# Kernel tuning notes

Hardware: AMD Instinct MI355X
Metric: run time of the kernel (lower is better)

## Reference

```python
import jax, jax.numpy as jnp
import numpy as np

IN_FEATURES = 4096
OUT_FEATURES = 4096
B, S = 4, 2048


def setup_inputs() -> dict:
    key = jax.random.key(0)
    k_x, k_w, k_ws, k_ss, k_b = jax.random.split(key, 5)
    x = jax.random.normal(k_x, (B, S, IN_FEATURES), dtype=jnp.float32)
    weight_quantized = jax.random.randint(k_w, (OUT_FEATURES, IN_FEATURES), -128, 128, dtype=jnp.int32).astype(jnp.int8)
    # realistic per-output-channel weight scales (small positive)
    weight_scale = jax.random.uniform(k_ws, (OUT_FEATURES,), dtype=jnp.float32, minval=1e-3, maxval=2e-2)
    # smoothing scales near 1 (clamped to [0.01, 100] in from_float)
    smooth_scale = jax.random.uniform(k_ss, (IN_FEATURES,), dtype=jnp.float32, minval=0.5, maxval=2.0)
    bias = 0.01 * jax.random.normal(k_b, (OUT_FEATURES,), dtype=jnp.float32)
    return {"x": x, "weight_quantized": weight_quantized, "weight_scale": weight_scale,
            "smooth_scale": smooth_scale, "bias": bias}


def reference(x, weight_quantized, weight_scale, smooth_scale, bias):
    # per-tensor dynamic activation quantization after smooth-scale divide
    x_smooth = x / smooth_scale                                   # [B,S,in]
    act_scale = jnp.max(jnp.abs(x_smooth)) / 127.0                # scalar
    x_quant = jnp.clip(jnp.round(x_smooth / (act_scale + 1e-5)), -128, 127).astype(jnp.int8)
    # int8 GEMM emulated in fp32 (matches torch reference: F.linear on float casts)
    out = jnp.einsum('bsi,oi->bso', x_quant.astype(jnp.float32),
                     weight_quantized.astype(jnp.float32))        # [B,S,out]
    out = out * act_scale * weight_scale                          # fused dequant
    return out + bias
```

## Files before the change

kernel.cpp:

```cpp
#include <hip/hip_runtime.h>
#include <stdint.h>

#define M_TOT 8192
#define N_TOT 4096
#define K_TOT 4096

typedef int v4i __attribute__((ext_vector_type(4)));

#define BM 256
#define BN 256
#define SUB 64
#define NS (K_TOT / SUB)
#define A_SUB (BM * SUB)
#define B_SUB (BN * SUB)
#define BUF_BYTES (A_SUB + B_SUB)

__global__ void prep_reduce(const int4* __restrict__ w32, int* __restrict__ w8,
                            int nw4, const float* __restrict__ smooth,
                            float* __restrict__ rcp, const float4* __restrict__ x,
                            unsigned int* __restrict__ maxbits, int nx4) {
  if (blockIdx.x == 0) {
    for (int i = threadIdx.x; i < K_TOT; i += blockDim.x) rcp[i] = 1.0f / smooth[i];
  }
  const int stride = gridDim.x * blockDim.x;
  const int g0 = blockIdx.x * blockDim.x + threadIdx.x;
  for (int i = g0; i < nw4; i += stride) {
    int4 v = w32[i];
    w8[i] = (v.x & 0xff) | ((v.y & 0xff) << 8) | ((v.z & 0xff) << 16) | (v.w << 24);
  }
  const float4* smooth4 = (const float4*)smooth;
  float m = 0.0f;
  for (int i = g0; i < nx4; i += stride) {
    float4 v = x[i];
    float4 s = smooth4[i & (K_TOT / 4 - 1)];
    m = fmaxf(m, fabsf(v.x / s.x));
    m = fmaxf(m, fabsf(v.y / s.y));
    m = fmaxf(m, fabsf(v.z / s.z));
    m = fmaxf(m, fabsf(v.w / s.w));
  }
#pragma unroll
  for (int off = 32; off; off >>= 1) m = fmaxf(m, __shfl_xor(m, off));
  __shared__ float sm[4];
  if ((threadIdx.x & 63) == 0) sm[threadIdx.x >> 6] = m;
  __syncthreads();
  if (threadIdx.x == 0) {
    float mm = fmaxf(fmaxf(sm[0], sm[1]), fmaxf(sm[2], sm[3]));
    atomicMax(maxbits, __float_as_uint(mm));
  }
}

__global__ void quantize_x(const float4* __restrict__ x,
                           const float4* __restrict__ rcp4,
                           const unsigned int* __restrict__ maxbits,
                           int* __restrict__ xq, int n4) {
  const float d = __uint_as_float(*maxbits) / 127.0f + 1e-5f;
  const float inv = 1.0f / d;
  int stride = gridDim.x * blockDim.x;
  for (int i = blockIdx.x * blockDim.x + threadIdx.x; i < n4; i += stride) {
    float4 v = x[i];
    float4 r = rcp4[i & (K_TOT / 4 - 1)];
    int q0 = (int)fminf(fmaxf(rintf(v.x * r.x * inv), -128.0f), 127.0f);
    int q1 = (int)fminf(fmaxf(rintf(v.y * r.y * inv), -128.0f), 127.0f);
    int q2 = (int)fminf(fmaxf(rintf(v.z * r.z * inv), -128.0f), 127.0f);
    int q3 = (int)fminf(fmaxf(rintf(v.w * r.w * inv), -128.0f), 127.0f);
    xq[i] = (q0 & 0xff) | ((q1 & 0xff) << 8) | ((q2 & 0xff) << 16) | (q3 << 24);
  }
}

__global__ __launch_bounds__(512, 2) void gemm_i8(
    const int8_t* __restrict__ Aq,
    const int8_t* __restrict__ Wt,
    const unsigned int* __restrict__ maxbits,
    const float* __restrict__ wscale,
    const float* __restrict__ bias,
    float* __restrict__ out) {
  __shared__ int8_t lds[4 * BUF_BYTES];

  const int tid = threadIdx.x;
  const int lane = tid & 63;
  const int wid = tid >> 6;
  const int l16 = lane & 15;
  const int lhi = lane >> 4;

  const int flat = blockIdx.y * gridDim.x + blockIdx.x;
  const int swz = (flat & 7) * 64 + (flat >> 3);
  const int m0 = (swz / (N_TOT / BN)) * BM;
  const int n0 = (swz % (N_TOT / BN)) * BN;

  const int wave_m = wid >> 2;
  const int wave_n = wid & 3;

  const int row_l = lane >> 2;
  const int gcol = ((lane & 3) ^ ((lane >> 3) & 3)) << 4;
  const int8_t* Abase = Aq + (size_t)m0 * K_TOT;
  const int8_t* Bbase = Wt + (size_t)n0 * K_TOT;
  int goff[2];
#pragma unroll
  for (int c = 0; c < 2; ++c) {
    int grow = (wid * 2 + c) * 16 + row_l;
    goff[c] = grow * K_TOT + gcol;
  }

  auto stage = [&](int dstbuf, int koff) {
#pragma unroll
    for (int c = 0; c < 2; ++c) {
      __builtin_amdgcn_global_load_lds(
          (const __attribute__((address_space(1))) void*)(Abase + goff[c] + koff),
          (__attribute__((address_space(3))) void*)(lds + dstbuf * BUF_BYTES + (wid * 2 + c) * 1024),
          16, 0, 0);
      __builtin_amdgcn_global_load_lds(
          (const __attribute__((address_space(1))) void*)(Bbase + goff[c] + koff),
          (__attribute__((address_space(3))) void*)(lds + dstbuf * BUF_BYTES + A_SUB + (wid * 2 + c) * 1024),
          16, 0, 0);
    }
  };

  const int slot = (lhi ^ ((l16 >> 1) & 3)) << 4;
  const int aOff = (wave_m * 128 + l16) * SUB + slot;
  const int bOff = (wave_n * 64 + l16) * SUB + slot;

  stage(0, 0);
  stage(1, SUB);
  stage(2, 2 * SUB);
  asm volatile("s_waitcnt vmcnt(8)" ::: "memory");
  __builtin_amdgcn_s_barrier();
  __builtin_amdgcn_sched_barrier(0);

  v4i acc[8][4] = {};

#pragma unroll 4
  for (int s = 0; s < NS; ++s) {
    const int buf = s & 3;
    const int8_t* Ab = lds + buf * BUF_BYTES;
    const int8_t* Bb = Ab + A_SUB;

    const int ts = (s + 3 < NS) ? (s + 3) : (NS - 1);
    stage((s + 3) & 3, ts * SUB);

    v4i a[8], b[4];
#pragma unroll
    for (int i = 0; i < 8; ++i) a[i] = *(const v4i*)(Ab + aOff + i * 1024);
#pragma unroll
    for (int j = 0; j < 4; ++j) b[j] = *(const v4i*)(Bb + bOff + j * 1024);

    __builtin_amdgcn_s_setprio(1);
#pragma unroll
    for (int i = 0; i < 8; ++i)
#pragma unroll
      for (int j = 0; j < 4; ++j)
        acc[i][j] = __builtin_amdgcn_mfma_i32_16x16x64_i8(a[i], b[j], acc[i][j], 0, 0, 0);
    __builtin_amdgcn_s_setprio(0);
    __builtin_amdgcn_sched_barrier(0);

    asm volatile("s_waitcnt lgkmcnt(0)" ::: "memory");
    asm volatile("s_waitcnt vmcnt(8)" ::: "memory");
    __builtin_amdgcn_sched_barrier(0);
    __builtin_amdgcn_s_barrier();
    __builtin_amdgcn_sched_barrier(0);
  }

  const float ascale = __uint_as_float(*maxbits) / 127.0f;
#pragma unroll
  for (int i = 0; i < 8; ++i) {
    const int orow = m0 + wave_m * 128 + i * 16 + lhi * 4;
#pragma unroll
    for (int j = 0; j < 4; ++j) {
      const int ocol = n0 + wave_n * 64 + j * 16 + l16;
      const float wsc = wscale[ocol] * ascale;
      const float bb = bias[ocol];
#pragma unroll
      for (int r = 0; r < 4; ++r) {
        out[(size_t)(orow + r) * N_TOT + ocol] = (float)acc[i][j][r] * wsc + bb;
      }
    }
  }
}

extern "C" void kernel_launch(void* const* d_in, const int* in_sizes, int n_in,
                              void* d_out, int out_size, void* d_ws, size_t ws_size,
                              hipStream_t stream) {
  const float* x = (const float*)d_in[0];
  const int* w32 = (const int*)d_in[1];
  const float* wscale = (const float*)d_in[2];
  const float* smooth = (const float*)d_in[3];
  const float* bias = (const float*)d_in[4];
  float* out = (float*)d_out;

  unsigned int* maxbits = (unsigned int*)d_ws;
  float* rcp = (float*)((char*)d_ws + 1024);
  int8_t* xq = (int8_t*)d_ws + (1 << 20);
  int8_t* wq8 = xq + (size_t)M_TOT * K_TOT;

  hipMemsetAsync(d_ws, 0, 4, stream);

  const int nw4 = N_TOT * K_TOT / 4;
  const int n4 = M_TOT * K_TOT / 4;
  prep_reduce<<<2048, 256, 0, stream>>>((const int4*)w32, (int*)wq8, nw4,
                                        smooth, rcp, (const float4*)x,
                                        maxbits, n4);
  quantize_x<<<2048, 256, 0, stream>>>((const float4*)x, (const float4*)rcp,
                                       maxbits, (int*)xq, n4);

  dim3 grid(N_TOT / BN, M_TOT / BM);
  gemm_i8<<<grid, 512, 0, stream>>>(xq, wq8, maxbits, wscale, bias, out);
}
```

Measured before the change: 224.9 us.

## Switch GEMM to 32x32x32 int8 MFMA and hoist smooth reciprocals per thread

The int8 GEMM now uses 32x32x32 MFMA instructions with 16-register accumulators in place of 16x16x64 tiles. Each wave issues fewer, larger MFMAs and reads A and B fragments as two k-halves per 64-wide sub-tile, with the epilogue store mapping adjusted to match. The prep and quantize kernels rely on the grid stride being a multiple of K/4, so each thread loads its smooth-scale values once, computes reciprocals up front, and drops the separate rcp buffer. Using a multiply by a reciprocal instead of a divide can change rounding near quantization boundaries, and the larger MFMA shape changes LDS read patterns and bank behaviour.

```diff
diff --git a/kernel.cpp b/kernel.cpp
--- a/kernel.cpp
+++ b/kernel.cpp
@@ -6,6 +6,7 @@
 #define K_TOT 4096
 
 typedef int v4i __attribute__((ext_vector_type(4)));
+typedef int v16i __attribute__((ext_vector_type(16)));
 
 #define BM 256
 #define BN 256
@@ -16,27 +17,24 @@
 #define BUF_BYTES (A_SUB + B_SUB)
 
 __global__ void prep_reduce(const int4* __restrict__ w32, int* __restrict__ w8,
-                            int nw4, const float* __restrict__ smooth,
-                            float* __restrict__ rcp, const float4* __restrict__ x,
+                            int nw4, const float4* __restrict__ smooth4,
+                            const float4* __restrict__ x,
                             unsigned int* __restrict__ maxbits, int nx4) {
-  if (blockIdx.x == 0) {
-    for (int i = threadIdx.x; i < K_TOT; i += blockDim.x) rcp[i] = 1.0f / smooth[i];
-  }
   const int stride = gridDim.x * blockDim.x;
   const int g0 = blockIdx.x * blockDim.x + threadIdx.x;
   for (int i = g0; i < nw4; i += stride) {
     int4 v = w32[i];
     w8[i] = (v.x & 0xff) | ((v.y & 0xff) << 8) | ((v.z & 0xff) << 16) | (v.w << 24);
   }
-  const float4* smooth4 = (const float4*)smooth;
+  float4 s = smooth4[g0 & (K_TOT / 4 - 1)];
+  const float rx = 1.0f / s.x, ry = 1.0f / s.y, rz = 1.0f / s.z, rw = 1.0f / s.w;
   float m = 0.0f;
   for (int i = g0; i < nx4; i += stride) {
     float4 v = x[i];
-    float4 s = smooth4[i & (K_TOT / 4 - 1)];
-    m = fmaxf(m, fabsf(v.x / s.x));
-    m = fmaxf(m, fabsf(v.y / s.y));
-    m = fmaxf(m, fabsf(v.z / s.z));
-    m = fmaxf(m, fabsf(v.w / s.w));
+    m = fmaxf(m, fabsf(v.x * rx));
+    m = fmaxf(m, fabsf(v.y * ry));
+    m = fmaxf(m, fabsf(v.z * rz));
+    m = fmaxf(m, fabsf(v.w * rw));
   }
 #pragma unroll
   for (int off = 32; off; off >>= 1) m = fmaxf(m, __shfl_xor(m, off));
@@ -50,19 +48,21 @@
 }
 
 __global__ void quantize_x(const float4* __restrict__ x,
-                           const float4* __restrict__ rcp4,
+                           const float4* __restrict__ smooth4,
                            const unsigned int* __restrict__ maxbits,
                            int* __restrict__ xq, int n4) {
   const float d = __uint_as_float(*maxbits) / 127.0f + 1e-5f;
   const float inv = 1.0f / d;
-  int stride = gridDim.x * blockDim.x;
-  for (int i = blockIdx.x * blockDim.x + threadIdx.x; i < n4; i += stride) {
+  const int stride = gridDim.x * blockDim.x;
+  const int g0 = blockIdx.x * blockDim.x + threadIdx.x;
+  float4 s = smooth4[g0 & (K_TOT / 4 - 1)];
+  const float rx = inv / s.x, ry = inv / s.y, rz = inv / s.z, rw = inv / s.w;
+  for (int i = g0; i < n4; i += stride) {
     float4 v = x[i];
-    float4 r = rcp4[i & (K_TOT / 4 - 1)];
-    int q0 = (int)fminf(fmaxf(rintf(v.x * r.x * inv), -128.0f), 127.0f);
-    int q1 = (int)fminf(fmaxf(rintf(v.y * r.y * inv), -128.0f), 127.0f);
-    int q2 = (int)fminf(fmaxf(rintf(v.z * r.z * inv), -128.0f), 127.0f);
-    int q3 = (int)fminf(fmaxf(rintf(v.w * r.w * inv), -128.0f), 127.0f);
+    int q0 = (int)fminf(fmaxf(rintf(v.x * rx), -128.0f), 127.0f);
+    int q1 = (int)fminf(fmaxf(rintf(v.y * ry), -128.0f), 127.0f);
+    int q2 = (int)fminf(fmaxf(rintf(v.z * rz), -128.0f), 127.0f);
+    int q3 = (int)fminf(fmaxf(rintf(v.w * rw), -128.0f), 127.0f);
     xq[i] = (q0 & 0xff) | ((q1 & 0xff) << 8) | ((q2 & 0xff) << 16) | (q3 << 24);
   }
 }
@@ -79,8 +79,8 @@
   const int tid = threadIdx.x;
   const int lane = tid & 63;
   const int wid = tid >> 6;
-  const int l16 = lane & 15;
-  const int lhi = lane >> 4;
+  const int l31 = lane & 31;
+  const int lhi5 = lane >> 5;
 
   const int flat = blockIdx.y * gridDim.x + blockIdx.x;
   const int swz = (flat & 7) * 64 + (flat >> 3);
@@ -115,9 +115,11 @@
     }
   };
 
-  const int slot = (lhi ^ ((l16 >> 1) & 3)) << 4;
-  const int aOff = (wave_m * 128 + l16) * SUB + slot;
-  const int bOff = (wave_n * 64 + l16) * SUB + slot;
+  const int f = (l31 >> 1) & 3;
+  const int slot0 = ((0 + lhi5) ^ f) << 4;
+  const int slot1 = ((2 + lhi5) ^ f) << 4;
+  const int aBase = (wave_m * 128 + l31) * SUB;
+  const int bBase = (wave_n * 64 + l31) * SUB;
 
   stage(0, 0);
   stage(1, SUB);
@@ -126,7 +128,7 @@
   __builtin_amdgcn_s_barrier();
   __builtin_amdgcn_sched_barrier(0);
 
-  v4i acc[8][4] = {};
+  v16i acc[4][2] = {};
 
 #pragma unroll 4
   for (int s = 0; s < NS; ++s) {
@@ -137,18 +139,29 @@
     const int ts = (s + 3 < NS) ? (s + 3) : (NS - 1);
     stage((s + 3) & 3, ts * SUB);
 
-    v4i a[8], b[4];
-#pragma unroll
-    for (int i = 0; i < 8; ++i) a[i] = *(const v4i*)(Ab + aOff + i * 1024);
-#pragma unroll
-    for (int j = 0; j < 4; ++j) b[j] = *(const v4i*)(Bb + bOff + j * 1024);
+    v4i a0[4], a1[4], b0[2], b1[2];
+#pragma unroll
+    for (int mf = 0; mf < 4; ++mf) {
+      a0[mf] = *(const v4i*)(Ab + aBase + mf * 2048 + slot0);
+      a1[mf] = *(const v4i*)(Ab + aBase + mf * 2048 + slot1);
+    }
+#pragma unroll
+    for (int nf = 0; nf < 2; ++nf) {
+      b0[nf] = *(const v4i*)(Bb + bBase + nf * 2048 + slot0);
+      b1[nf] = *(const v4i*)(Bb + bBase + nf * 2048 + slot1);
+    }
 
     __builtin_amdgcn_s_setprio(1);
 #pragma unroll
-    for (int i = 0; i < 8; ++i)
-#pragma unroll
-      for (int j = 0; j < 4; ++j)
-        acc[i][j] = __builtin_amdgcn_mfma_i32_16x16x64_i8(a[i], b[j], acc[i][j], 0, 0, 0);
+    for (int mf = 0; mf < 4; ++mf)
+#pragma unroll
+      for (int nf = 0; nf < 2; ++nf)
+        acc[mf][nf] = __builtin_amdgcn_mfma_i32_32x32x32_i8(a0[mf], b0[nf], acc[mf][nf], 0, 0, 0);
+#pragma unroll
+    for (int mf = 0; mf < 4; ++mf)
+#pragma unroll
+      for (int nf = 0; nf < 2; ++nf)
+        acc[mf][nf] = __builtin_amdgcn_mfma_i32_32x32x32_i8(a1[mf], b1[nf], acc[mf][nf], 0, 0, 0);
     __builtin_amdgcn_s_setprio(0);
     __builtin_amdgcn_sched_barrier(0);
 
@@ -161,16 +174,17 @@
 
   const float ascale = __uint_as_float(*maxbits) / 127.0f;
 #pragma unroll
-  for (int i = 0; i < 8; ++i) {
-    const int orow = m0 + wave_m * 128 + i * 16 + lhi * 4;
-#pragma unroll
-    for (int j = 0; j < 4; ++j) {
-      const int ocol = n0 + wave_n * 64 + j * 16 + l16;
+  for (int mf = 0; mf < 4; ++mf) {
+#pragma unroll
+    for (int nf = 0; nf < 2; ++nf) {
+      const int ocol = n0 + wave_n * 64 + nf * 32 + l31;
       const float wsc = wscale[ocol] * ascale;
       const float bb = bias[ocol];
-#pragma unroll
-      for (int r = 0; r < 4; ++r) {
-        out[(size_t)(orow + r) * N_TOT + ocol] = (float)acc[i][j][r] * wsc + bb;
+      const int rbase = m0 + wave_m * 128 + mf * 32 + 4 * lhi5;
+#pragma unroll
+      for (int reg = 0; reg < 16; ++reg) {
+        const int orow = rbase + (reg & 3) + 8 * (reg >> 2);
+        out[(size_t)orow * N_TOT + ocol] = (float)acc[mf][nf][reg] * wsc + bb;
       }
     }
   }
@@ -187,7 +201,6 @@
   float* out = (float*)d_out;
 
   unsigned int* maxbits = (unsigned int*)d_ws;
-  float* rcp = (float*)((char*)d_ws + 1024);
   int8_t* xq = (int8_t*)d_ws + (1 << 20);
   int8_t* wq8 = xq + (size_t)M_TOT * K_TOT;
 
@@ -196,9 +209,9 @@
   const int nw4 = N_TOT * K_TOT / 4;
   const int n4 = M_TOT * K_TOT / 4;
   prep_reduce<<<2048, 256, 0, stream>>>((const int4*)w32, (int*)wq8, nw4,
-                                        smooth, rcp, (const float4*)x,
+                                        (const float4*)smooth, (const float4*)x,
                                         maxbits, n4);
-  quantize_x<<<2048, 256, 0, stream>>>((const float4*)x, (const float4*)rcp,
+  quantize_x<<<2048, 256, 0, stream>>>((const float4*)x, (const float4*)smooth,
                                        maxbits, (int*)xq, n4);
 
   dim3 grid(N_TOT / BN, M_TOT / BM);
```

Measured after the change: 239.0 us. 6.3% more time.

## Fuse max-reduction and activation quantization into one cooperative kernel

Applied to the files above, without the earlier changes.

Merges the reduce kernel and the quantize kernel into a single cooperative launch that uses a grid-wide sync between the abs-max reduction and the quantization pass. Because the grid stride is a multiple of K/4, each thread's smooth-scale column is fixed, so reciprocals and the combined quantization factor are computed once per thread instead of dividing per element. This removes one kernel launch and the separate rcp buffer, and makes the second read of x more likely to hit in cache. In exchange it depends on cooperative launch support and a grid barrier, and uses a smaller grid of 1024 blocks.

```diff
diff --git a/kernel.cpp b/kernel.cpp
--- a/kernel.cpp
+++ b/kernel.cpp
@@ -1,5 +1,8 @@
 #include <hip/hip_runtime.h>
+#include <hip/hip_cooperative_groups.h>
 #include <stdint.h>
+
+namespace cg = cooperative_groups;
 
 #define M_TOT 8192
 #define N_TOT 4096
@@ -15,28 +18,26 @@
 #define B_SUB (BN * SUB)
 #define BUF_BYTES (A_SUB + B_SUB)
 
-__global__ void prep_reduce(const int4* __restrict__ w32, int* __restrict__ w8,
-                            int nw4, const float* __restrict__ smooth,
-                            float* __restrict__ rcp, const float4* __restrict__ x,
-                            unsigned int* __restrict__ maxbits, int nx4) {
-  if (blockIdx.x == 0) {
-    for (int i = threadIdx.x; i < K_TOT; i += blockDim.x) rcp[i] = 1.0f / smooth[i];
-  }
+__global__ void prep_all(const int4* __restrict__ w32, int* __restrict__ w8,
+                         int nw4, const float4* __restrict__ smooth4,
+                         const float4* __restrict__ x,
+                         unsigned int* __restrict__ maxbits, int nx4,
+                         int* __restrict__ xq) {
   const int stride = gridDim.x * blockDim.x;
   const int g0 = blockIdx.x * blockDim.x + threadIdx.x;
   for (int i = g0; i < nw4; i += stride) {
     int4 v = w32[i];
     w8[i] = (v.x & 0xff) | ((v.y & 0xff) << 8) | ((v.z & 0xff) << 16) | (v.w << 24);
   }
-  const float4* smooth4 = (const float4*)smooth;
+  float4 s = smooth4[g0 & (K_TOT / 4 - 1)];
+  const float rx = 1.0f / s.x, ry = 1.0f / s.y, rz = 1.0f / s.z, rw = 1.0f / s.w;
   float m = 0.0f;
   for (int i = g0; i < nx4; i += stride) {
     float4 v = x[i];
-    float4 s = smooth4[i & (K_TOT / 4 - 1)];
-    m = fmaxf(m, fabsf(v.x / s.x));
-    m = fmaxf(m, fabsf(v.y / s.y));
-    m = fmaxf(m, fabsf(v.z / s.z));
-    m = fmaxf(m, fabsf(v.w / s.w));
+    m = fmaxf(m, fabsf(v.x * rx));
+    m = fmaxf(m, fabsf(v.y * ry));
+    m = fmaxf(m, fabsf(v.z * rz));
+    m = fmaxf(m, fabsf(v.w * rw));
   }
 #pragma unroll
   for (int off = 32; off; off >>= 1) m = fmaxf(m, __shfl_xor(m, off));
@@ -46,23 +47,23 @@
   if (threadIdx.x == 0) {
     float mm = fmaxf(fmaxf(sm[0], sm[1]), fmaxf(sm[2], sm[3]));
     atomicMax(maxbits, __float_as_uint(mm));
-  }
-}
-
-__global__ void quantize_x(const float4* __restrict__ x,
-                           const float4* __restrict__ rcp4,
-                           const unsigned int* __restrict__ maxbits,
-                           int* __restrict__ xq, int n4) {
-  const float d = __uint_as_float(*maxbits) / 127.0f + 1e-5f;
-  const float inv = 1.0f / d;
-  int stride = gridDim.x * blockDim.x;
-  for (int i = blockIdx.x * blockDim.x + threadIdx.x; i < n4; i += stride) {
+    __threadfence();
+  }
+  cg::this_grid().sync();
+  __shared__ float s_inv;
+  if (threadIdx.x == 0) {
+    unsigned mb = atomicOr(maxbits, 0u);
+    s_inv = 1.0f / (__uint_as_float(mb) / 127.0f + 1e-5f);
+  }
+  __syncthreads();
+  const float inv = s_inv;
+  const float qx = inv / s.x, qy = inv / s.y, qz = inv / s.z, qw = inv / s.w;
+  for (int i = g0; i < nx4; i += stride) {
     float4 v = x[i];
-    float4 r = rcp4[i & (K_TOT / 4 - 1)];
-    int q0 = (int)fminf(fmaxf(rintf(v.x * r.x * inv), -128.0f), 127.0f);
-    int q1 = (int)fminf(fmaxf(rintf(v.y * r.y * inv), -128.0f), 127.0f);
-    int q2 = (int)fminf(fmaxf(rintf(v.z * r.z * inv), -128.0f), 127.0f);
-    int q3 = (int)fminf(fmaxf(rintf(v.w * r.w * inv), -128.0f), 127.0f);
+    int q0 = (int)fminf(fmaxf(rintf(v.x * qx), -128.0f), 127.0f);
+    int q1 = (int)fminf(fmaxf(rintf(v.y * qy), -128.0f), 127.0f);
+    int q2 = (int)fminf(fmaxf(rintf(v.z * qz), -128.0f), 127.0f);
+    int q3 = (int)fminf(fmaxf(rintf(v.w * qw), -128.0f), 127.0f);
     xq[i] = (q0 & 0xff) | ((q1 & 0xff) << 8) | ((q2 & 0xff) << 16) | (q3 << 24);
   }
 }
@@ -187,19 +188,21 @@
   float* out = (float*)d_out;
 
   unsigned int* maxbits = (unsigned int*)d_ws;
-  float* rcp = (float*)((char*)d_ws + 1024);
   int8_t* xq = (int8_t*)d_ws + (1 << 20);
   int8_t* wq8 = xq + (size_t)M_TOT * K_TOT;
 
   hipMemsetAsync(d_ws, 0, 4, stream);
 
-  const int nw4 = N_TOT * K_TOT / 4;
-  const int n4 = M_TOT * K_TOT / 4;
-  prep_reduce<<<2048, 256, 0, stream>>>((const int4*)w32, (int*)wq8, nw4,
-                                        smooth, rcp, (const float4*)x,
-                                        maxbits, n4);
-  quantize_x<<<2048, 256, 0, stream>>>((const float4*)x, (const float4*)rcp,
-                                       maxbits, (int*)xq, n4);
+  int nw4 = N_TOT * K_TOT / 4;
+  int n4 = M_TOT * K_TOT / 4;
+  const int4* w32v = (const int4*)w32;
+  int* wq8v = (int*)wq8;
+  const float4* smooth4 = (const float4*)smooth;
+  const float4* x4 = (const float4*)x;
+  int* xqv = (int*)xq;
+  void* args[] = {(void*)&w32v, (void*)&wq8v, (void*)&nw4, (void*)&smooth4,
+                  (void*)&x4, (void*)&maxbits, (void*)&n4, (void*)&xqv};
+  hipLaunchCooperativeKernel((void*)prep_all, dim3(1024), dim3(256), args, 0, stream);
 
   dim3 grid(N_TOT / BN, M_TOT / BM);
   gemm_i8<<<grid, 512, 0, stream>>>(xq, wq8, maxbits, wscale, bias, out);
```

After: 319.7 us. +42.1%, slower.
